# Kernel tuning notes

Hardware: AMD Instinct MI355X
Metric: run time of the kernel (lower is better)

Reference implementation:

```python
import jax, jax.numpy as jnp
import numpy as np
import math

B, S, D_IN, D_OUT, H = 2, 2048, 1024, 1024, 16
HD = D_OUT // H


def setup_inputs() -> dict:
    key = jax.random.key(0)
    ks = jax.random.split(key, 6)
    scale = 0.02
    return {
        "x": jax.random.normal(ks[0], (B, S, D_IN), dtype=jnp.float32),
        "Wq": jax.random.normal(ks[1], (D_IN, D_OUT), dtype=jnp.float32) * scale,
        "Wk": jax.random.normal(ks[2], (D_IN, D_OUT), dtype=jnp.float32) * scale,
        "Wv": jax.random.normal(ks[3], (D_IN, D_OUT), dtype=jnp.float32) * scale,
        "Wo": jax.random.normal(ks[4], (D_OUT, D_OUT), dtype=jnp.float32) * scale,
        "bo": jax.random.normal(ks[5], (D_OUT,), dtype=jnp.float32) * scale,
    }


def reference(x, Wq, Wk, Wv, Wo, bo):
    b, n, _ = x.shape
    # project and split heads -> [b, h, n, hd]
    q = (x @ Wq).reshape(b, n, H, HD).transpose(0, 2, 1, 3)
    k = (x @ Wk).reshape(b, n, H, HD).transpose(0, 2, 1, 3)
    v = (x @ Wv).reshape(b, n, H, HD).transpose(0, 2, 1, 3)
    # materialized [b, h, n, n] scores with causal mask (as in original)
    scores = jnp.einsum('bhqd,bhkd->bhqk', q, k)
    causal = jnp.tril(jnp.ones((n, n), dtype=bool))  # True = keep
    scores = jnp.where(causal, scores, -jnp.inf)
    attn = jax.nn.softmax(scores / math.sqrt(HD), axis=-1)
    ctx = jnp.einsum('bhqk,bhkd->bhqd', attn, v)
    ctx = ctx.transpose(0, 2, 1, 3).reshape(b, n, D_OUT)
    return ctx @ Wo + bo
```

## Files before the change

### kernel.cpp

```cpp
#include <hip/hip_runtime.h>
#include <hip/hip_bf16.h>
#include <math.h>

typedef __bf16 v8bf __attribute__((ext_vector_type(8)));
typedef __bf16 v4bf __attribute__((ext_vector_type(4)));
typedef short  v4s  __attribute__((ext_vector_type(4)));
typedef float  v4f  __attribute__((ext_vector_type(4)));
typedef unsigned short u16;

static_assert(sizeof(v8bf) == 16, "v8bf must be 16B");

__device__ __forceinline__ u16 f2bf(float f) {
  __hip_bfloat16 h = __float2bfloat16(f);
  return *reinterpret_cast<u16*>(&h);
}
__device__ __forceinline__ v4f mfma16(v8bf a, v8bf b, v4f c) {
  return __builtin_amdgcn_mfma_f32_16x16x32_bf16(a, b, c, 0, 0, 0);
}
__device__ __forceinline__ v4f mfma16k16(v4bf a, v4bf b, v4f c) {
#if __has_builtin(__builtin_amdgcn_mfma_f32_16x16x16_bf16)
  return __builtin_amdgcn_mfma_f32_16x16x16_bf16(a, b, c, 0, 0, 0);
#else
  union { v4bf f; v4s s; } ua, ub;
  ua.f = a; ub.f = b;
  return __builtin_amdgcn_mfma_f32_16x16x16bf16_1k(ua.s, ub.s, c, 0, 0, 0);
#endif
}
__device__ __forceinline__ void async16(const u16* g, u16* l) {
  __builtin_amdgcn_global_load_lds(
      (__attribute__((address_space(1))) void*)(void*)g,
      (__attribute__((address_space(3))) void*)l, 16, 0, 0);
}

__global__ void prep(const float* __restrict__ x, const float* __restrict__ Wq,
                     const float* __restrict__ Wk, const float* __restrict__ Wv,
                     const float* __restrict__ Wo, u16* __restrict__ Wt,
                     u16* __restrict__ xb) {
  int tx = threadIdx.x, ty = threadIdx.y;
  if (blockIdx.z == 4) {
    int bid = blockIdx.y * 32 + blockIdx.x;
    int i = (bid * 1024 + ty * 32 + tx) * 4;
    float4 v = *(const float4*)(x + i);
    ushort4 o;
    o.x = f2bf(v.x); o.y = f2bf(v.y); o.z = f2bf(v.z); o.w = f2bf(v.w);
    *(ushort4*)(xb + i) = o;
    return;
  }
  __shared__ float tile[32][33];
  const float* src = (blockIdx.z == 0) ? Wq : (blockIdx.z == 1) ? Wk : (blockIdx.z == 2) ? Wv : Wo;
  int k0 = blockIdx.x * 32, n0 = blockIdx.y * 32;
  tile[ty][tx] = src[(size_t)(k0 + ty) * 1024 + n0 + tx];
  __syncthreads();
  Wt[(size_t)(blockIdx.z * 1024 + n0 + ty) * 1024 + k0 + tx] = f2bf(tile[tx][ty]);
}

__device__ __forceinline__ void gemm_core(const u16* __restrict__ A, const u16* __restrict__ Bt,
                                          u16* sA, u16* sB, v4f acc[4][4], int bm, int bn) {
  const int t = threadIdx.x;
  const int w = t >> 6, l = t & 63;
  const int quad = l >> 4, low = l & 15;
  const int wm = (w & 1) * 64, wn = (w >> 1) * 64;
  const int rowA = bm * 128 + w * 32 + (l >> 2);
  const int rowB = bn * 128 + w * 32 + (l >> 2);
  const int col8 = (l & 3) * 8;

  auto STAGE = [&](int kb, int bi) {
    u16* la = sA + bi * 4096 + w * 1024;
    u16* lb = sB + bi * 4096 + w * 1024;
    async16(A + (size_t)rowA * 1024 + kb + col8, la);
    async16(A + (size_t)(rowA + 16) * 1024 + kb + col8, la + 512);
    async16(Bt + (size_t)rowB * 1024 + kb + col8, lb);
    async16(Bt + (size_t)(rowB + 16) * 1024 + kb + col8, lb + 512);
  };

  STAGE(0, 0);
  asm volatile("s_waitcnt vmcnt(0)" ::: "memory");
  __builtin_amdgcn_s_barrier();
  int cur = 0;
  for (int kb = 0; kb < 1024; kb += 32) {
    if (kb + 32 < 1024) STAGE(kb + 32, cur ^ 1);
    const u16* pa = sA + cur * 4096;
    const u16* pb = sB + cur * 4096;
    v8bf af[4], bfr[4];
#pragma unroll
    for (int i = 0; i < 4; i++)
      af[i] = *(const v8bf*)(pa + (wm + i * 16 + low) * 32 + quad * 8);
#pragma unroll
    for (int j = 0; j < 4; j++)
      bfr[j] = *(const v8bf*)(pb + (wn + j * 16 + low) * 32 + quad * 8);
#pragma unroll
    for (int i = 0; i < 4; i++)
#pragma unroll
      for (int j = 0; j < 4; j++)
        acc[i][j] = mfma16(af[i], bfr[j], acc[i][j]);
    asm volatile("s_waitcnt vmcnt(0)" ::: "memory");
    __builtin_amdgcn_s_barrier();
    cur ^= 1;
  }
}

__global__ __launch_bounds__(256) void gemm_qkv(const u16* __restrict__ xb,
                                                const u16* __restrict__ Wt,
                                                u16* __restrict__ Qb,
                                                u16* __restrict__ Kb,
                                                u16* __restrict__ Vt) {
  __shared__ __align__(16) u16 sA[2 * 128 * 32];
  __shared__ __align__(16) u16 sB[2 * 128 * 32];
  v4f acc[4][4] = {};
  const int bm = blockIdx.x, bn = blockIdx.y;
  gemm_core(xb, Wt, sA, sB, acc, bm, bn);
  const int t = threadIdx.x, w = t >> 6, l = t & 63, quad = l >> 4, low = l & 15;
  const int wm = (w & 1) * 64, wn = (w >> 1) * 64;
  const int zone = (bn * 128) >> 10;
  const float qsc = (zone == 0) ? 0.18033688011112042f : 1.0f;
#pragma unroll
  for (int i = 0; i < 4; i++) {
    int m0 = bm * 128 + wm + i * 16 + quad * 4;
#pragma unroll
    for (int j = 0; j < 4; j++) {
      int nn = (bn * 128 + wn + j * 16 + low) & 1023;
      if (zone == 0) {
#pragma unroll
        for (int r = 0; r < 4; r++)
          Qb[(size_t)(m0 + r) * 1024 + nn] = f2bf(acc[i][j][r] * qsc);
      } else if (zone == 1) {
#pragma unroll
        for (int r = 0; r < 4; r++)
          Kb[(size_t)(m0 + r) * 1024 + nn] = f2bf(acc[i][j][r]);
      } else {
        int bb = m0 >> 11, s = m0 & 2047;
#pragma unroll
        for (int r = 0; r < 4; r++)
          Vt[(size_t)(bb * 1024 + nn) * 2048 + s + r] = f2bf(acc[i][j][r]);
      }
    }
  }
}

__global__ __launch_bounds__(256) void gemm_out(const u16* __restrict__ ctx,
                                                const u16* __restrict__ Wt,
                                                const float* __restrict__ bo,
                                                float* __restrict__ out) {
  __shared__ __align__(16) u16 sA[2 * 128 * 32];
  __shared__ __align__(16) u16 sB[2 * 64 * 32];
  const u16* Bt = Wt + (size_t)3072 * 1024;
  v4f acc[4][2] = {};
  const int bm = blockIdx.x, bn = blockIdx.y;
  const int t = threadIdx.x, w = t >> 6, l = t & 63, quad = l >> 4, low = l & 15;
  const int wm = (w & 1) * 64, wn = (w >> 1) * 32;
  const int rowA = bm * 128 + w * 32 + (l >> 2);
  const int rowB = bn * 64 + w * 16 + (l >> 2);
  const int col8 = (l & 3) * 8;

  auto STAGE = [&](int kb, int bi) {
    u16* la = sA + bi * 4096 + w * 1024;
    u16* lb = sB + bi * 2048 + w * 512;
    async16(ctx + (size_t)rowA * 1024 + kb + col8, la);
    async16(ctx + (size_t)(rowA + 16) * 1024 + kb + col8, la + 512);
    async16(Bt + (size_t)rowB * 1024 + kb + col8, lb);
  };

  STAGE(0, 0);
  asm volatile("s_waitcnt vmcnt(0)" ::: "memory");
  __builtin_amdgcn_s_barrier();
  int cur = 0;
  for (int kb = 0; kb < 1024; kb += 32) {
    if (kb + 32 < 1024) STAGE(kb + 32, cur ^ 1);
    const u16* pa = sA + cur * 4096;
    const u16* pb = sB + cur * 2048;
    v8bf af[4], bfr[2];
#pragma unroll
    for (int i = 0; i < 4; i++)
      af[i] = *(const v8bf*)(pa + (wm + i * 16 + low) * 32 + quad * 8);
#pragma unroll
    for (int j = 0; j < 2; j++)
      bfr[j] = *(const v8bf*)(pb + (wn + j * 16 + low) * 32 + quad * 8);
#pragma unroll
    for (int i = 0; i < 4; i++)
#pragma unroll
      for (int j = 0; j < 2; j++)
        acc[i][j] = mfma16(af[i], bfr[j], acc[i][j]);
    asm volatile("s_waitcnt vmcnt(0)" ::: "memory");
    __builtin_amdgcn_s_barrier();
    cur ^= 1;
  }
#pragma unroll
  for (int i = 0; i < 4; i++) {
    int m0 = bm * 128 + wm + i * 16 + quad * 4;
#pragma unroll
    for (int j = 0; j < 2; j++) {
      int n = bn * 64 + wn + j * 16 + low;
      float bias = bo[n];
#pragma unroll
      for (int r = 0; r < 4; r++)
        out[(size_t)(m0 + r) * 1024 + n] = acc[i][j][r] + bias;
    }
  }
}

__global__ __launch_bounds__(256) void attn(const u16* __restrict__ Qb,
                                            const u16* __restrict__ Kb,
                                            const u16* __restrict__ Vt,
                                            u16* __restrict__ ctx) {
  __shared__ __align__(16) u16 sK[4][4096];
  __shared__ __align__(16) u16 sV[4][4096];
  const int t = threadIdx.x, w = t >> 6, l = t & 63, quad = l >> 4, low = l & 15;

  const int bid = blockIdx.x;
  const int xcd = bid & 7, slot = bid >> 3;
  const int pair = xcd * 4 + (slot & 3);
  const int tp = slot >> 2;
  const int b = pair >> 4, h = pair & 15;

  const u16* kbase = Kb + (size_t)(b * 2048) * 1024 + h * 64;
  const u16* vbase = Vt + (size_t)(b * 1024 + h * 64) * 2048;

  const int srow = l >> 3;
  const int cg = (l & 7) ^ srow;

  auto STAGE = [&](int tt, int bi) {
    const int kb = tt * 64;
    const u16* kg = kbase + (size_t)(kb + w * 8 + srow) * 1024 + cg * 8;
    async16(kg, &sK[bi][w * 512]);
    async16(kg + (size_t)32 * 1024, &sK[bi][2048 + w * 512]);
    const u16* vg = vbase + (size_t)(w * 8 + srow) * 2048 + kb + cg * 8;
    async16(vg, &sV[bi][w * 512]);
    async16(vg + (size_t)32 * 2048, &sV[bi][2048 + w * 512]);
  };

  for (int ph = 0; ph < 2; ++ph) {
    const int tile = ph ? tp : 31 - tp;
    const int nkt = tile + 1;
    const int qw = tile * 64 + w * 16;

    if (ph) {
      asm volatile("s_waitcnt lgkmcnt(0)" ::: "memory");
      __builtin_amdgcn_s_barrier();
    }

    const u16* qrow_p = Qb + (size_t)(b * 2048 + qw + low) * 1024 + h * 64;
    v8bf qa0 = *(const v8bf*)(qrow_p + quad * 8);
    v8bf qa1 = *(const v8bf*)(qrow_p + 32 + quad * 8);
    asm volatile("" ::: "memory");

    float li = 0.f;
    v4f o[4] = {};

    STAGE(0, 0);
    if (nkt > 1) STAGE(1, 1);

    for (int it = 0; it < nkt; ++it) {
      const int bi = it & 3;
      if (it + 2 < nkt) STAGE(it + 2, (it + 2) & 3);
      asm volatile("s_waitcnt lgkmcnt(0)" ::: "memory");
      const int c = nkt - 1 - it;
      if (c >= 2)      asm volatile("s_waitcnt vmcnt(8)" ::: "memory");
      else if (c == 1) asm volatile("s_waitcnt vmcnt(4)" ::: "memory");
      else             asm volatile("s_waitcnt vmcnt(0)" ::: "memory");
      __builtin_amdgcn_s_barrier();

      const int kb = it * 64;
      v4f s[4] = {};
      __builtin_amdgcn_s_setprio(1);
#pragma unroll
      for (int cf = 0; cf < 4; cf++) {
        const int key = cf * 16 + low;
        v8bf kf0 = *(const v8bf*)(&sK[bi][key * 64 + ((quad ^ (key & 7)) * 8)]);
        v8bf kf1 = *(const v8bf*)(&sK[bi][key * 64 + (((4 + quad) ^ (key & 7)) * 8)]);
        s[cf] = mfma16(kf0, qa0, s[cf]);
        s[cf] = mfma16(kf1, qa1, s[cf]);
      }
      __builtin_amdgcn_s_setprio(0);

      const bool dm = (it == nkt - 1);
      const int qr = qw + low;
      v4bf pf[4];
#pragma unroll
      for (int cf = 0; cf < 4; cf++)
#pragma unroll
        for (int r = 0; r < 4; r++) {
          float e = __builtin_amdgcn_exp2f(s[cf][r]);
          if (dm && (kb + cf * 16 + quad * 4 + r > qr)) e = 0.f;
          li += e;
          pf[cf][r] = (__bf16)e;
        }

      __builtin_amdgcn_s_setprio(1);
#pragma unroll
      for (int df = 0; df < 4; df++) {
        const int d = df * 16 + low;
#pragma unroll
        for (int cf = 0; cf < 4; cf++) {
          const int c2 = cf * 2 + (quad >> 1);
          const v4bf vf = *(const v4bf*)(&sV[bi][d * 64 + ((c2 ^ (d & 7)) * 8) + (quad & 1) * 4]);
          o[df] = mfma16k16(pf[cf], vf, o[df]);
        }
      }
      __builtin_amdgcn_s_setprio(0);
    }

    li += __shfl_xor(li, 16);
    li += __shfl_xor(li, 32);

#pragma unroll
    for (int r = 0; r < 4; r++) {
      float lir = __shfl(li, quad * 4 + r);
      float inv = 1.f / lir;
      int row = b * 2048 + qw + quad * 4 + r;
#pragma unroll
      for (int df = 0; df < 4; df++)
        ctx[(size_t)row * 1024 + h * 64 + df * 16 + low] = f2bf(o[df][r] * inv);
    }
  }
}

extern "C" void kernel_launch(void* const* d_in, const int* in_sizes, int n_in,
                              void* d_out, int out_size, void* d_ws, size_t ws_size,
                              hipStream_t stream) {
  const float* x  = (const float*)d_in[0];
  const float* Wq = (const float*)d_in[1];
  const float* Wk = (const float*)d_in[2];
  const float* Wv = (const float*)d_in[3];
  const float* Wo = (const float*)d_in[4];
  const float* bo = (const float*)d_in[5];
  float* out = (float*)d_out;

  char* ws = (char*)d_ws;
  u16* xb  = (u16*)(ws);
  u16* Wt  = (u16*)(ws + 8ull * 1024 * 1024);
  u16* Qb  = (u16*)(ws + 16ull * 1024 * 1024);
  u16* Kb  = (u16*)(ws + 24ull * 1024 * 1024);
  u16* Vt  = (u16*)(ws + 32ull * 1024 * 1024);
  u16* ctx = (u16*)(ws + 40ull * 1024 * 1024);

  prep<<<dim3(32, 32, 5), dim3(32, 32, 1), 0, stream>>>(x, Wq, Wk, Wv, Wo, Wt, xb);
  gemm_qkv<<<dim3(32, 24, 1), dim3(256, 1, 1), 0, stream>>>(xb, Wt, Qb, Kb, Vt);
  attn<<<dim3(512, 1, 1), dim3(256, 1, 1), 0, stream>>>(Qb, Kb, Vt, ctx);
  gemm_out<<<dim3(32, 16, 1), dim3(256, 1, 1), 0, stream>>>(ctx, Wt, bo, out);
}
```

Baseline: 179.1 us.

## Deepen GEMM async-copy pipeline to four LDS buffers with prefetch distance two

```diff
diff --git a/kernel.cpp b/kernel.cpp
--- a/kernel.cpp
+++ b/kernel.cpp
@@ -74,13 +74,19 @@
   };
 
   STAGE(0, 0);
-  asm volatile("s_waitcnt vmcnt(0)" ::: "memory");
-  __builtin_amdgcn_s_barrier();
-  int cur = 0;
-  for (int kb = 0; kb < 1024; kb += 32) {
-    if (kb + 32 < 1024) STAGE(kb + 32, cur ^ 1);
-    const u16* pa = sA + cur * 4096;
-    const u16* pb = sB + cur * 4096;
+  STAGE(32, 1);
+  for (int it = 0; it < 32; ++it) {
+    const int bi = it & 3;
+    if (it + 2 < 32) STAGE((it + 2) * 32, (it + 2) & 3);
+    asm volatile("s_waitcnt lgkmcnt(0)" ::: "memory");
+    const int c = 31 - it;
+    if (c >= 2)      asm volatile("s_waitcnt vmcnt(8)" ::: "memory");
+    else if (c == 1) asm volatile("s_waitcnt vmcnt(4)" ::: "memory");
+    else             asm volatile("s_waitcnt vmcnt(0)" ::: "memory");
+    __builtin_amdgcn_s_barrier();
+
+    const u16* pa = sA + bi * 4096;
+    const u16* pb = sB + bi * 4096;
     v8bf af[4], bfr[4];
 #pragma unroll
     for (int i = 0; i < 4; i++)
@@ -88,14 +94,13 @@
 #pragma unroll
     for (int j = 0; j < 4; j++)
       bfr[j] = *(const v8bf*)(pb + (wn + j * 16 + low) * 32 + quad * 8);
+    __builtin_amdgcn_s_setprio(1);
 #pragma unroll
     for (int i = 0; i < 4; i++)
 #pragma unroll
       for (int j = 0; j < 4; j++)
         acc[i][j] = mfma16(af[i], bfr[j], acc[i][j]);
-    asm volatile("s_waitcnt vmcnt(0)" ::: "memory");
-    __builtin_amdgcn_s_barrier();
-    cur ^= 1;
+    __builtin_amdgcn_s_setprio(0);
   }
 }
 
@@ -104,8 +109,8 @@
                                                 u16* __restrict__ Qb,
                                                 u16* __restrict__ Kb,
                                                 u16* __restrict__ Vt) {
-  __shared__ __align__(16) u16 sA[2 * 128 * 32];
-  __shared__ __align__(16) u16 sB[2 * 128 * 32];
+  __shared__ __align__(16) u16 sA[4 * 128 * 32];
+  __shared__ __align__(16) u16 sB[4 * 128 * 32];
   v4f acc[4][4] = {};
   const int bm = blockIdx.x, bn = blockIdx.y;
   gemm_core(xb, Wt, sA, sB, acc, bm, bn);
@@ -141,8 +146,8 @@
                                                 const u16* __restrict__ Wt,
                                                 const float* __restrict__ bo,
                                                 float* __restrict__ out) {
-  __shared__ __align__(16) u16 sA[2 * 128 * 32];
-  __shared__ __align__(16) u16 sB[2 * 64 * 32];
+  __shared__ __align__(16) u16 sA[4 * 128 * 32];
+  __shared__ __align__(16) u16 sB[4 * 64 * 32];
   const u16* Bt = Wt + (size_t)3072 * 1024;
   v4f acc[4][2] = {};
   const int bm = blockIdx.x, bn = blockIdx.y;
@@ -161,13 +166,19 @@
   };
 
   STAGE(0, 0);
-  asm volatile("s_waitcnt vmcnt(0)" ::: "memory");
-  __builtin_amdgcn_s_barrier();
-  int cur = 0;
-  for (int kb = 0; kb < 1024; kb += 32) {
-    if (kb + 32 < 1024) STAGE(kb + 32, cur ^ 1);
-    const u16* pa = sA + cur * 4096;
-    const u16* pb = sB + cur * 2048;
+  STAGE(32, 1);
+  for (int it = 0; it < 32; ++it) {
+    const int bi = it & 3;
+    if (it + 2 < 32) STAGE((it + 2) * 32, (it + 2) & 3);
+    asm volatile("s_waitcnt lgkmcnt(0)" ::: "memory");
+    const int c = 31 - it;
+    if (c >= 2)      asm volatile("s_waitcnt vmcnt(6)" ::: "memory");
+    else if (c == 1) asm volatile("s_waitcnt vmcnt(3)" ::: "memory");
+    else             asm volatile("s_waitcnt vmcnt(0)" ::: "memory");
+    __builtin_amdgcn_s_barrier();
+
+    const u16* pa = sA + bi * 4096;
+    const u16* pb = sB + bi * 2048;
     v8bf af[4], bfr[2];
 #pragma unroll
     for (int i = 0; i < 4; i++)
@@ -175,14 +186,13 @@
 #pragma unroll
     for (int j = 0; j < 2; j++)
       bfr[j] = *(const v8bf*)(pb + (wn + j * 16 + low) * 32 + quad * 8);
+    __builtin_amdgcn_s_setprio(1);
 #pragma unroll
     for (int i = 0; i < 4; i++)
 #pragma unroll
       for (int j = 0; j < 2; j++)
         acc[i][j] = mfma16(af[i], bfr[j], acc[i][j]);
-    asm volatile("s_waitcnt vmcnt(0)" ::: "memory");
-    __builtin_amdgcn_s_barrier();
-    cur ^= 1;
+    __builtin_amdgcn_s_setprio(0);
   }
 #pragma unroll
   for (int i = 0; i < 4; i++) {
```

New measurement: 184.3 us. 2.9% more time.
